# Kernel tuning notes

Measured on AMD Instinct MI355X. Metric: run time of the kernel, lower is better.

## Reference

```python
import jax, jax.numpy as jnp
import numpy as np

B, K, R, H, S = 4, 64, 16, 16, 2048


def setup_inputs() -> dict:
    key = jax.random.key(0)
    k1, k2, k3 = jax.random.split(key, 3)
    adj_matrix = jax.random.normal(k1, (B, K, K, R), dtype=jnp.float32)
    relation_head_weights = jax.random.normal(k2, (R, H), dtype=jnp.float32) * 0.02
    top_k_indices = jax.random.randint(k3, (B, K), 0, S)
    return {
        "adj_matrix": adj_matrix,
        "relation_head_weights": relation_head_weights,
        "top_k_indices": top_k_indices,
        "seq_l": S,
    }


def reference(adj_matrix, relation_head_weights, top_k_indices, seq_l):
    # adj_matrix: [B, K, K, R], relation_head_weights: [R, H]
    num_heads = relation_head_weights.shape[1]
    k = adj_matrix.shape[1]
    # head_adj: [B, H, K, K]
    head_adj = jnp.einsum('bijr,rh->bhij', adj_matrix, relation_head_weights)
    # mean over source dim (dim=2 of [B,H,K,K]) -> anchor_salience [B, H, K]
    anchor_salience = head_adj.mean(axis=2)

    def scatter_one(anchor_b, idx):
        # anchor_b: [H, K], idx: [K]
        # full_bias[:, :, idx] = anchor_b[:, None, :] broadcast over rows
        vals = jnp.broadcast_to(anchor_b[:, None, :], (num_heads, seq_l, k))
        return jnp.zeros((num_heads, seq_l, seq_l), dtype=adj_matrix.dtype).at[:, :, idx].set(vals)

    return jax.vmap(scatter_one)(anchor_salience, top_k_indices)  # [B, H, S, S]
```

## Files before the change

### kernel.cpp

```cpp
#include <hip/hip_runtime.h>

#define B_ 4
#define K_ 64
#define R_ 16
#define H_ 16
#define S_ 2048
#define ROWS_PER_BLOCK 16

__global__ __launch_bounds__(256) void compute_colval_kernel(
    const float* __restrict__ adj,
    const float* __restrict__ W,
    const int*   __restrict__ idx,
    float*       __restrict__ colval)
{
    __shared__ float s_jr[K_ * R_];
    __shared__ float s_anchor[H_ * K_];
    __shared__ float s_W[R_ * H_];

    const int b   = blockIdx.x;
    const int tid = threadIdx.x;

    if (tid < R_ * H_) s_W[tid] = W[tid];

    float4* cv4 = reinterpret_cast<float4*>(colval + (size_t)b * H_ * S_);
    #pragma unroll
    for (int i = tid; i < (H_ * S_) / 4; i += 256) {
        cv4[i] = make_float4(0.f, 0.f, 0.f, 0.f);
    }

    const float* adjb = adj + (size_t)b * K_ * K_ * R_;
    float acc0 = 0.f, acc1 = 0.f, acc2 = 0.f, acc3 = 0.f;
    for (int i = 0; i < K_; ++i) {
        const float* row = adjb + i * (K_ * R_);
        acc0 += row[tid];
        acc1 += row[tid + 256];
        acc2 += row[tid + 512];
        acc3 += row[tid + 768];
    }
    s_jr[tid]       = acc0;
    s_jr[tid + 256] = acc1;
    s_jr[tid + 512] = acc2;
    s_jr[tid + 768] = acc3;
    __syncthreads();

    for (int p = tid; p < H_ * K_; p += 256) {
        const int h = p >> 6;
        const int j = p & 63;
        float a = 0.f;
        #pragma unroll
        for (int r = 0; r < R_; ++r)
            a += s_jr[j * R_ + r] * s_W[r * H_ + h];
        s_anchor[p] = a * (1.0f / K_);
    }
    __syncthreads();

    if (tid < H_) {
        const int h = tid;
        float* cvh = colval + ((size_t)b * H_ + h) * S_;
        for (int k = 0; k < K_; ++k) {
            const int c = idx[b * K_ + k];
            cvh[c] = s_anchor[h * K_ + k];
        }
    }
}

__global__ __launch_bounds__(256) void broadcast_rows_kernel(
    const float4* __restrict__ colval4,
    float4*       __restrict__ out4)
{
    const int bh   = blockIdx.y;
    const int row0 = blockIdx.x * ROWS_PER_BLOCK;
    const int t    = threadIdx.x;

    const int cvbase = bh * (S_ / 4);
    const float4 v0 = colval4[cvbase + t];
    const float4 v1 = colval4[cvbase + 256 + t];

    float4* base = out4 + ((size_t)bh * S_ + row0) * (S_ / 4);
    #pragma unroll
    for (int r = 0; r < ROWS_PER_BLOCK; ++r) {
        base[(size_t)r * (S_ / 4) + t]       = v0;
        base[(size_t)r * (S_ / 4) + 256 + t] = v1;
    }
}

extern "C" void kernel_launch(void* const* d_in, const int* in_sizes, int n_in,
                              void* d_out, int out_size, void* d_ws, size_t ws_size,
                              hipStream_t stream) {
    const float* adj = (const float*)d_in[0];
    const float* W   = (const float*)d_in[1];
    const int*   idx = (const int*)d_in[2];

    float* out    = (float*)d_out;
    float* colval = (float*)d_ws;

    compute_colval_kernel<<<B_, 256, 0, stream>>>(adj, W, idx, colval);

    dim3 grid(S_ / ROWS_PER_BLOCK, B_ * H_);
    broadcast_rows_kernel<<<grid, 256, 0, stream>>>(
        (const float4*)colval, (float4*)out);
}
```

Before: 202.6 us.

## Split adjacency reduction across more blocks and use nontemporal output stores

Replaces the 4-block serial reduction over 64 source rows with a two-stage reduction: 64 blocks each sum 4 rows into partials, then a finalize kernel sums 16 partials per batch before the head projection and scatter. This spreads the reduction across many more CUs instead of four. The broadcast kernel now writes the large output with nontemporal stores to avoid polluting cache. The cost is an extra kernel launch and a partial buffer in workspace.

```diff
diff --git a/kernel.cpp b/kernel.cpp
--- a/kernel.cpp
+++ b/kernel.cpp
@@ -6,9 +6,29 @@
 #define H_ 16
 #define S_ 2048
 #define ROWS_PER_BLOCK 16
+#define NCH 16
+#define IPB 4
 
-__global__ __launch_bounds__(256) void compute_colval_kernel(
-    const float* __restrict__ adj,
+typedef float f32x4 __attribute__((ext_vector_type(4)));
+
+__global__ __launch_bounds__(256) void partial_reduce_kernel(
+    const f32x4* __restrict__ adj4,
+    f32x4*       __restrict__ partial4)
+{
+    const int b   = blockIdx.x;
+    const int ch  = blockIdx.y;
+    const int tid = threadIdx.x;
+
+    const f32x4* base = adj4 + ((size_t)b * K_ + ch * IPB) * (K_ * R_ / 4);
+    f32x4 acc = (f32x4)(0.f);
+    #pragma unroll
+    for (int i = 0; i < IPB; ++i)
+        acc += base[i * (K_ * R_ / 4) + tid];
+    partial4[((size_t)b * NCH + ch) * 256 + tid] = acc;
+}
+
+__global__ __launch_bounds__(256) void finalize_colval_kernel(
+    const f32x4* __restrict__ partial4,
     const float* __restrict__ W,
     const int*   __restrict__ idx,
     float*       __restrict__ colval)
@@ -22,25 +42,17 @@
 
     if (tid < R_ * H_) s_W[tid] = W[tid];
 
-    float4* cv4 = reinterpret_cast<float4*>(colval + (size_t)b * H_ * S_);
+    f32x4* cv4 = reinterpret_cast<f32x4*>(colval + (size_t)b * H_ * S_);
     #pragma unroll
-    for (int i = tid; i < (H_ * S_) / 4; i += 256) {
-        cv4[i] = make_float4(0.f, 0.f, 0.f, 0.f);
-    }
+    for (int i = tid; i < (H_ * S_) / 4; i += 256)
+        cv4[i] = (f32x4)(0.f);
 
-    const float* adjb = adj + (size_t)b * K_ * K_ * R_;
-    float acc0 = 0.f, acc1 = 0.f, acc2 = 0.f, acc3 = 0.f;
-    for (int i = 0; i < K_; ++i) {
-        const float* row = adjb + i * (K_ * R_);
-        acc0 += row[tid];
-        acc1 += row[tid + 256];
-        acc2 += row[tid + 512];
-        acc3 += row[tid + 768];
-    }
-    s_jr[tid]       = acc0;
-    s_jr[tid + 256] = acc1;
-    s_jr[tid + 512] = acc2;
-    s_jr[tid + 768] = acc3;
+    const f32x4* pb = partial4 + (size_t)b * NCH * 256;
+    f32x4 acc = (f32x4)(0.f);
+    #pragma unroll
+    for (int c = 0; c < NCH; ++c)
+        acc += pb[c * 256 + tid];
+    reinterpret_cast<f32x4*>(s_jr)[tid] = acc;
     __syncthreads();
 
     for (int p = tid; p < H_ * K_; p += 256) {
@@ -65,22 +77,22 @@
 }
 
 __global__ __launch_bounds__(256) void broadcast_rows_kernel(
-    const float4* __restrict__ colval4,
-    float4*       __restrict__ out4)
+    const f32x4* __restrict__ colval4,
+    f32x4*       __restrict__ out4)
 {
     const int bh   = blockIdx.y;
     const int row0 = blockIdx.x * ROWS_PER_BLOCK;
     const int t    = threadIdx.x;
 
     const int cvbase = bh * (S_ / 4);
-    const float4 v0 = colval4[cvbase + t];
-    const float4 v1 = colval4[cvbase + 256 + t];
+    const f32x4 v0 = colval4[cvbase + t];
+    const f32x4 v1 = colval4[cvbase + 256 + t];
 
-    float4* base = out4 + ((size_t)bh * S_ + row0) * (S_ / 4);
+    f32x4* base = out4 + ((size_t)bh * S_ + row0) * (S_ / 4);
     #pragma unroll
     for (int r = 0; r < ROWS_PER_BLOCK; ++r) {
-        base[(size_t)r * (S_ / 4) + t]       = v0;
-        base[(size_t)r * (S_ / 4) + 256 + t] = v1;
+        __builtin_nontemporal_store(v0, &base[(size_t)r * (S_ / 4) + t]);
+        __builtin_nontemporal_store(v1, &base[(size_t)r * (S_ / 4) + 256 + t]);
     }
 }
 
@@ -91,12 +103,18 @@
     const float* W   = (const float*)d_in[1];
     const int*   idx = (const int*)d_in[2];
 
-    float* out    = (float*)d_out;
-    float* colval = (float*)d_ws;
+    float* out     = (float*)d_out;
+    float* colval  = (float*)d_ws;
+    float* partial = colval + (size_t)B_ * H_ * S_;
 
-    compute_colval_kernel<<<B_, 256, 0, stream>>>(adj, W, idx, colval);
+    dim3 gA1(B_, NCH);
+    partial_reduce_kernel<<<gA1, 256, 0, stream>>>(
+        (const f32x4*)adj, (f32x4*)partial);
 
-    dim3 grid(S_ / ROWS_PER_BLOCK, B_ * H_);
-    broadcast_rows_kernel<<<grid, 256, 0, stream>>>(
-        (const float4*)colval, (float4*)out);
+    finalize_colval_kernel<<<B_, 256, 0, stream>>>(
+        (const f32x4*)partial, W, idx, colval);
+
+    dim3 gB(S_ / ROWS_PER_BLOCK, B_ * H_);
+    broadcast_rows_kernel<<<gB, 256, 0, stream>>>(
+        (const f32x4*)colval, (f32x4*)out);
 }
```

Measured after the change: 207.9 us. +2.6%, slower.
